# Kernel optimization log

Hardware: AMD Instinct MI355X
Metric: run time of the kernel (lower is better)

Reference implementation:

```python
import jax, jax.numpy as jnp
import numpy as np

B, S, D = 4, 2048, 512

def setup_inputs() -> dict:
    key = jax.random.key(0)
    ks = jax.random.split(key, 7)
    # scale weights so unscaled logits stay in a sane softmax range
    w_scale = 0.05
    return {
        "x": jax.random.normal(ks[0], (B, S, D), dtype=jnp.float32),
        "W_q": jax.random.normal(ks[1], (D, D), dtype=jnp.float32) * w_scale,
        "W_k": jax.random.normal(ks[2], (D, D), dtype=jnp.float32) * w_scale,
        "W_v": jax.random.normal(ks[3], (D, D), dtype=jnp.float32) * w_scale,
        "b_q": jax.random.normal(ks[4], (D,), dtype=jnp.float32) * w_scale,
        "b_k": jax.random.normal(ks[5], (D,), dtype=jnp.float32) * w_scale,
        "b_v": jax.random.normal(ks[6], (D,), dtype=jnp.float32) * w_scale,
    }

def reference(x, W_q, W_k, W_v, b_q, b_k, b_v):
    # QKV projections: [B,S,D] @ [D,D] + [D]
    q = jnp.einsum('bsd,de->bse', x, W_q) + b_q
    k = jnp.einsum('bsd,de->bse', x, W_k) + b_k
    v = jnp.einsum('bsd,de->bse', x, W_v) + b_v
    # unscaled attention scores [B,S,S]
    scores = jnp.einsum('bqd,bkd->bqk', q, k)
    attn = jax.nn.softmax(scores, axis=-1)
    # weighted sum of values [B,S,D]
    return jnp.einsum('bqk,bkd->bqd', attn, v)
```

## Files before the change

kernel.cpp:

```cpp
#include <hip/hip_runtime.h>
#include <hip/hip_bf16.h>
#include <hip/hip_fp16.h>

#define BB 4
#define SS 2048
#define DD 512

typedef short s16x8 __attribute__((ext_vector_type(8)));
typedef short s16x4 __attribute__((ext_vector_type(4)));
typedef float f32x4 __attribute__((ext_vector_type(4)));
typedef _Float16 f16x8 __attribute__((ext_vector_type(8)));

__device__ __forceinline__ short f2h(float f) {
    const _Float16 h = (_Float16)f;
    union { _Float16 h; short s; } u; u.h = h; return u.s;
}
__device__ __forceinline__ f16x8 as_h(s16x8 v) {
    union { s16x8 s; f16x8 h; } u; u.s = v; return u.h;
}

__device__ __forceinline__ void gload_lds16(const void* g, void* l) {
    __builtin_amdgcn_global_load_lds(
        (const __attribute__((address_space(1))) void*)g,
        (__attribute__((address_space(3))) void*)l, 16, 0, 0);
}

#define SB0 __builtin_amdgcn_sched_barrier(0)
#define LGKM0 asm volatile("s_waitcnt lgkmcnt(0)" ::: "memory")
#define VM0   asm volatile("s_waitcnt vmcnt(0)" ::: "memory")

__global__ __launch_bounds__(256, 4) void qkt128(
    const short* __restrict__ qf, const short* __restrict__ kf,
    short* __restrict__ outS, int nwg)
{
    __shared__ short lds[16384];

    const int tid = threadIdx.x;
    const int wave = tid >> 6, lane = tid & 63;
    const int flat = blockIdx.x + 16 * blockIdx.y + 256 * blockIdx.z;
    const int w = (flat & 7) * (nwg >> 3) + (flat >> 3);
    const int bm = ((w >> 4) & 15) * 128, bn = (w & 15) * 128;
    const long z = w >> 8;
    qf += z * (long)SS * DD; kf += z * (long)SS * DD;
    outS += z * (long)SS * SS;

    const int wm = (wave >> 1) * 64, wn = (wave & 1) * 64;
    const int lrow = lane & 15, lk16 = (lane >> 4) * 16;

    f32x4 acc[4][4] = {};

    auto base = [&](int buf, int arr) -> short* { return &lds[(buf * 2 + arr) * 4096]; };
    auto issue = [&](int buf, int arr, int k0) {
#pragma unroll
        for (int h = 0; h < 2; h++) {
            const int Lb = (h << 12) + (tid << 4);
            const int Ls = Lb ^ (((Lb >> 7) & 3) << 4);
            const int row = Ls >> 6, elem = (Ls & 63) >> 1;
            const short* s = arr ? kf : qf;
            const int rb = arr ? bn : bm;
            gload_lds16(s + (size_t)(rb + row) * DD + k0 + elem,
                        (char*)base(buf, arr) + Lb);
        }
    };
    auto rd = [&](int buf, int arr, int row) -> s16x8 {
        const int L = (row << 6) + lk16;
        const int Ls = L ^ (((L >> 7) & 3) << 4);
        return *(const s16x8*)((const char*)base(buf, arr) + Ls);
    };

#define QK_TILE(T, CUR, PREF)                                                    \
  {                                                                              \
    s16x8 a[4], b[4];                                                            \
    _Pragma("unroll")                                                            \
    for (int m = 0; m < 4; m++) a[m] = rd(CUR, 0, wm + m * 16 + lrow);           \
    _Pragma("unroll")                                                            \
    for (int n = 0; n < 4; n++) b[n] = rd(CUR, 1, wn + n * 16 + lrow);           \
    if (PREF) { issue((CUR) ^ 1, 1, ((T) + 1) * 32); SB0;                        \
                issue((CUR) ^ 1, 0, ((T) + 1) * 32); }                           \
    LGKM0; SB0;                                                                  \
    __builtin_amdgcn_s_setprio(1);                                               \
    _Pragma("unroll")                                                            \
    for (int m = 0; m < 4; m++) {                                                \
      _Pragma("unroll")                                                          \
      for (int n = 0; n < 4; n++)                                                \
        acc[m][n] = __builtin_amdgcn_mfma_f32_16x16x32_f16(                      \
            as_h(a[m]), as_h(b[n]), acc[m][n], 0, 0, 0);                         \
    }                                                                            \
    __builtin_amdgcn_s_setprio(0);                                               \
    if (PREF) { VM0; SB0; }                                                      \
    __builtin_amdgcn_s_barrier();                                                \
  }

    issue(0, 1, 0); issue(0, 0, 0);
    VM0;
    __builtin_amdgcn_s_barrier();

    for (int t = 0; t < 16; t += 2) {
        QK_TILE(t,     0, 1);
        QK_TILE(t + 1, 1, (t + 1) < 15);
    }
#undef QK_TILE

    __syncthreads();
    short* ebuf = &lds[0];
#pragma unroll
    for (int m = 0; m < 4; m++) {
#pragma unroll
        for (int n = 0; n < 4; n++) {
#pragma unroll
            for (int j = 0; j < 4; j++) {
                const int rl = wm + m * 16 + (lane >> 4) * 4 + j;
                const int cl = wn + n * 16 + lrow;
                ebuf[rl * 128 + (cl ^ ((rl & 7) << 3))] =
                    (short)__float2int_rn(acc[m][n][j] * 128.0f);
            }
        }
    }
    __syncthreads();
#pragma unroll
    for (int it = 0; it < 8; it++) {
        const int u = it * 256 + tid;
        const int r = u >> 4, c8 = (u & 15) * 8;
        const s16x8 val = *(const s16x8*)&ebuf[r * 128 + (c8 ^ ((r & 7) << 3))];
        *(s16x8*)&outS[(size_t)(bm + r) * SS + bn + c8] = val;
    }
}

__global__ __launch_bounds__(256, 4) void proj_all(
    const short* __restrict__ xh, const short* __restrict__ wt,
    const float* __restrict__ bq, const float* __restrict__ bk,
    const float* __restrict__ bv,
    short* __restrict__ qfp, short* __restrict__ kfp, short* __restrict__ vt)
{
    __shared__ short lds[16384];

    const int tid = threadIdx.x;
    const int wave = tid >> 6, lane = tid & 63;
    const int flat = blockIdx.x + 12 * blockIdx.y;
    const int w = (flat & 7) * 96 + (flat >> 3);
    const int bxi = w % 12, byi = w / 12;
    const int wsel = bxi >> 2;
    const int bnl = (bxi & 3) * 128;
    const int bm = byi * 128;
    const short* B0 = wt + (size_t)wsel * DD * DD;
    const float* bias = (wsel == 0) ? bq : (wsel == 1) ? bk : bv;

    f32x4 acc[4][4] = {};
    const int wm = (wave >> 1) * 64, wn = (wave & 1) * 64;
    const int lrow = lane & 15, lk16 = (lane >> 4) * 16;

    auto base = [&](int buf, int arr) -> short* { return &lds[(buf * 2 + arr) * 4096]; };
    auto issue = [&](int buf, int arr, int k0) {
#pragma unroll
        for (int h = 0; h < 2; h++) {
            const int Lb = (h << 12) + (tid << 4);
            const int Ls = Lb ^ (((Lb >> 7) & 3) << 4);
            const int row = Ls >> 6, elem = (Ls & 63) >> 1;
            const short* s = arr ? B0 : xh;
            const int rb = arr ? bnl : bm;
            gload_lds16(s + (size_t)(rb + row) * DD + k0 + elem,
                        (char*)base(buf, arr) + Lb);
        }
    };
    auto rd = [&](int buf, int arr, int row) -> s16x8 {
        const int L = (row << 6) + lk16;
        const int Ls = L ^ (((L >> 7) & 3) << 4);
        return *(const s16x8*)((const char*)base(buf, arr) + Ls);
    };

#define PJ_TILE(T, CUR, PREF)                                                    \
  {                                                                              \
    s16x8 a[4], b[4];                                                            \
    _Pragma("unroll")                                                            \
    for (int m = 0; m < 4; m++) a[m] = rd(CUR, 0, wm + m * 16 + lrow);           \
    _Pragma("unroll")                                                            \
    for (int n = 0; n < 4; n++) b[n] = rd(CUR, 1, wn + n * 16 + lrow);           \
    if (PREF) { issue((CUR) ^ 1, 1, ((T) + 1) * 32); SB0;                        \
                issue((CUR) ^ 1, 0, ((T) + 1) * 32); }                           \
    LGKM0; SB0;                                                                  \
    __builtin_amdgcn_s_setprio(1);                                               \
    _Pragma("unroll")                                                            \
    for (int m = 0; m < 4; m++) {                                                \
      _Pragma("unroll")                                                          \
      for (int n = 0; n < 4; n++)                                                \
        acc[m][n] = __builtin_amdgcn_mfma_f32_16x16x32_f16(                      \
            as_h(a[m]), as_h(b[n]), acc[m][n], 0, 0, 0);                         \
    }                                                                            \
    __builtin_amdgcn_s_setprio(0);                                               \
    if (PREF) { VM0; SB0; }                                                      \
    __builtin_amdgcn_s_barrier();                                                \
  }

    issue(0, 1, 0); issue(0, 0, 0);
    VM0;
    __builtin_amdgcn_s_barrier();

    for (int t = 0; t < 16; t += 2) {
        PJ_TILE(t,     0, 1);
        PJ_TILE(t + 1, 1, (t + 1) < 15);
    }
#undef PJ_TILE

    __syncthreads();
    short* cbuf = &lds[0];
#pragma unroll
    for (int m = 0; m < 4; m++) {
#pragma unroll
        for (int n = 0; n < 4; n++) {
#pragma unroll
            for (int j = 0; j < 4; j++) {
                const int rl = wm + m * 16 + (lane >> 4) * 4 + j;
                const int cl = wn + n * 16 + lrow;
                const float v = acc[m][n][j] + bias[bnl + cl];
                if (wsel < 2)
                    cbuf[rl * 128 + (cl ^ ((rl & 7) << 3))] = f2h(v);
                else
                    cbuf[cl * 128 + (rl ^ ((cl & 7) << 3))] = f2h(v);
            }
        }
    }
    __syncthreads();
    if (wsel < 2) {
        short* outp = wsel ? kfp : qfp;
#pragma unroll
        for (int it = 0; it < 8; it++) {
            const int u = it * 256 + tid;
            const int r = u >> 4, c8 = (u & 15) * 8;
            const s16x8 val = *(const s16x8*)&cbuf[r * 128 + (c8 ^ ((r & 7) << 3))];
            *(s16x8*)&outp[(size_t)(bm + r) * DD + bnl + c8] = val;
        }
    } else {
        const int b = bm >> 11, s0 = bm & 2047;
#pragma unroll
        for (int it = 0; it < 8; it++) {
            const int idx = it * 256 + tid;
            const int dd = idx >> 4, c8 = (idx & 15) * 8;
            const s16x8 val = *(const s16x8*)&cbuf[dd * 128 + (c8 ^ ((dd & 7) << 3))];
            *(s16x8*)&vt[((size_t)b << 20) + ((size_t)(bnl + dd) << 11) + s0 + c8] = val;
        }
    }
}

__global__ __launch_bounds__(256, 3) void pv_gemm(
    const short* __restrict__ P, const short* __restrict__ vt,
    float* __restrict__ out, int nwg)
{
    __shared__ short As[2][64 * 64];
    __shared__ short Bs[2][128 * 64];

    const int tid = threadIdx.x;
    const int wave = tid >> 6, lane = tid & 63;
    const int flat = blockIdx.x + 4 * blockIdx.y + 128 * blockIdx.z;
    const int w = (flat & 7) * (nwg >> 3) + (flat >> 3);
    const int bm = ((w >> 2) & 31) * 64, bn = (w & 3) * 128;
    const long z = w >> 7;
    P += z * (long)SS * SS;
    vt += z << 20;
    out += z * (long)SS * DD;

    f32x4 acc[2][4] = {};
    const int wm = (wave >> 1) * 32, wn = (wave & 1) * 64;
    const int lrow = lane & 15, lk = (lane >> 4) * 8;

    auto swz = [](int L) { return L ^ (((L >> 7) & 7) << 4); };
    auto issueA = [&](int buf, int k0) {
#pragma unroll
        for (int h = 0; h < 2; h++) {
            const int L = (h << 12) + (tid << 4);
            const int Ls = swz(L);
            const int row = Ls >> 7, col = (Ls & 127) >> 1;
            gload_lds16(P + (size_t)(bm + row) * SS + k0 + col, (char*)&As[buf][0] + L);
        }
    };
    auto issueB = [&](int buf, int k0) {
#pragma unroll
        for (int h = 0; h < 4; h++) {
            const int L = (h << 12) + (tid << 4);
            const int Ls = swz(L);
            const int row = Ls >> 7, col = (Ls & 127) >> 1;
            gload_lds16(vt + ((size_t)(bn + row) << 11) + k0 + col, (char*)&Bs[buf][0] + L);
        }
    };

#define PV_TILE(T, CUR, PREF)                                                    \
  {                                                                              \
    s16x8 a[2][2], b[2][4];                                                      \
    _Pragma("unroll")                                                            \
    for (int kx = 0; kx < 2; kx++) {                                             \
      _Pragma("unroll")                                                          \
      for (int m = 0; m < 2; m++)                                                \
        a[kx][m] = *(const s16x8*)((const char*)&As[CUR][0] +                    \
                   swz(((wm + m * 16 + lrow) * 64 + kx * 32 + lk) * 2));         \
      _Pragma("unroll")                                                          \
      for (int n = 0; n < 4; n++)                                                \
        b[kx][n] = *(const s16x8*)((const char*)&Bs[CUR][0] +                    \
                   swz(((wn + n * 16 + lrow) * 64 + kx * 32 + lk) * 2));         \
    }                                                                            \
    if (PREF) { issueB((CUR) ^ 1, ((T) + 1) * 64); SB0;                          \
                issueA((CUR) ^ 1, ((T) + 1) * 64); }                             \
    LGKM0; SB0;                                                                  \
    __builtin_amdgcn_s_setprio(1);                                               \
    _Pragma("unroll")                                                            \
    for (int kx = 0; kx < 2; kx++) {                                             \
      _Pragma("unroll")                                                          \
      for (int m = 0; m < 2; m++) {                                              \
        _Pragma("unroll")                                                        \
        for (int n = 0; n < 4; n++)                                              \
          acc[m][n] = __builtin_amdgcn_mfma_f32_16x16x32_f16(                    \
              as_h(a[kx][m]), as_h(b[kx][n]), acc[m][n], 0, 0, 0);               \
      }                                                                          \
    }                                                                            \
    __builtin_amdgcn_s_setprio(0);                                               \
    if (PREF) { VM0; SB0; }                                                      \
    __builtin_amdgcn_s_barrier();                                                \
  }

    issueB(0, 0); issueA(0, 0);
    VM0;
    __builtin_amdgcn_s_barrier();

    for (int t = 0; t < 32; t += 2) {
        PV_TILE(t,     0, 1);
        PV_TILE(t + 1, 1, (t + 1) < 31);
    }
#undef PV_TILE

#pragma unroll
    for (int m = 0; m < 2; m++) {
#pragma unroll
        for (int n = 0; n < 4; n++) {
#pragma unroll
            for (int j = 0; j < 4; j++) {
                const int row = bm + wm + m * 16 + (lane >> 4) * 4 + j;
                const int col = bn + wn + n * 16 + lrow;
                out[(size_t)row * DD + col] = acc[m][n][j];
            }
        }
    }
}

__global__ __launch_bounds__(256) void cast_all(
    const float* __restrict__ x,
    const float* __restrict__ wq, const float* __restrict__ wk,
    const float* __restrict__ wv,
    short* __restrict__ xh, short* __restrict__ wt)
{
    const int bid = blockIdx.x;
    if (bid < 4096) {
        const int i = bid * 256 + threadIdx.x;
        const float4 v = ((const float4*)x)[i];
        const float vv[4] = {v.x, v.y, v.z, v.w};
        s16x4 h;
#pragma unroll
        for (int j = 0; j < 4; j++) h[j] = f2h(vv[j]);
        ((s16x4*)xh)[i] = h;
    } else {
        const int t = (bid - 4096) * 256 + threadIdx.x;
        const int w = t >> 18;
        const int r = t & 262143;
        const float* src = (w == 0) ? wq : ((w == 1) ? wk : wv);
        const float v = src[r];
        const int k = r >> 9, n = r & 511;
        wt[((size_t)w << 18) + ((size_t)n << 9) + k] = f2h(v);
    }
}

__global__ __launch_bounds__(256) void softmax_rows(
    const short* __restrict__ S, short* __restrict__ P)
{
    const int row = blockIdx.x;
    const long z = blockIdx.y;
    const short* s = S + z * (long)SS * SS + (long)row * SS;
    short* p = P + z * (long)SS * SS + (long)row * SS;
    const int tid = threadIdx.x;

    const s16x8 raw = ((const s16x8*)s)[tid];
    float v[8];
#pragma unroll
    for (int j = 0; j < 8; j++) v[j] = (float)(int)raw[j] * 0.0078125f;

    float m = v[0];
#pragma unroll
    for (int j = 1; j < 8; j++) m = fmaxf(m, v[j]);
#pragma unroll
    for (int off = 32; off >= 1; off >>= 1) m = fmaxf(m, __shfl_xor(m, off));
    __shared__ float redm[4], reds[4];
    if ((tid & 63) == 0) redm[tid >> 6] = m;
    __syncthreads();
    m = fmaxf(fmaxf(redm[0], redm[1]), fmaxf(redm[2], redm[3]));

    float e[8], sum = 0.f;
#pragma unroll
    for (int j = 0; j < 8; j++) { e[j] = __expf(v[j] - m); sum += e[j]; }
#pragma unroll
    for (int off = 32; off >= 1; off >>= 1) sum += __shfl_xor(sum, off);
    if ((tid & 63) == 0) reds[tid >> 6] = sum;
    __syncthreads();
    sum = reds[0] + reds[1] + reds[2] + reds[3];
    const float inv = 1.0f / sum;

    s16x8 o;
#pragma unroll
    for (int j = 0; j < 8; j++) o[j] = f2h(e[j] * inv);
    ((s16x8*)p)[tid] = o;
}

extern "C" void kernel_launch(void* const* d_in, const int* in_sizes, int n_in,
                              void* d_out, int out_size, void* d_ws, size_t ws_size,
                              hipStream_t stream)
{
    const float* x  = (const float*)d_in[0];
    const float* Wq = (const float*)d_in[1];
    const float* Wk = (const float*)d_in[2];
    const float* Wv = (const float*)d_in[3];
    const float* bq = (const float*)d_in[4];
    const float* bk = (const float*)d_in[5];
    const float* bv = (const float*)d_in[6];
    float* out = (float*)d_out;

    const size_t MK = (size_t)BB * SS * DD;
    char* ws = (char*)d_ws;
    short* xh  = (short*)ws; ws += MK * 2;
    short* wt  = (short*)ws; ws += 3ull * DD * DD * 2;
    short* qfp = (short*)ws; ws += MK * 2;
    short* kfp = (short*)ws; ws += MK * 2;
    short* vt  = (short*)ws; ws += MK * 2;
    const size_t fixed = (size_t)(ws - (char*)d_ws);

    int g = 4;
    while (g > 0 && fixed + (size_t)g * ((size_t)SS * SS * 2 + (size_t)SS * SS * 2) > ws_size)
        g >>= 1;
    if (g == 0) return;
    short* sc = (short*)ws;
    short* P  = (short*)(ws + (size_t)g * SS * SS * 2);

    cast_all<<<dim3(7168), 256, 0, stream>>>(x, Wq, Wk, Wv, xh, wt);
    proj_all<<<dim3(12, 64), 256, 0, stream>>>(xh, wt, bq, bk, bv,
                                               qfp, kfp, vt);

    for (int b0 = 0; b0 < BB; b0 += g) {
        const int gg = (b0 + g <= BB) ? g : (BB - b0);
        qkt128<<<dim3(16, 16, gg), 256, 0, stream>>>(
            qfp + (size_t)b0 * SS * DD, kfp + (size_t)b0 * SS * DD, sc, 256 * gg);
        softmax_rows<<<dim3(SS, gg), 256, 0, stream>>>(sc, P);
        pv_gemm<<<dim3(4, 32, gg), 256, 0, stream>>>(
            P, vt + ((size_t)b0 << 20), out + (size_t)b0 * SS * DD, 128 * gg);
    }
}
```

Before: 100.9 us.

## Triple-buffer LDS tiles in QK^T and projection GEMMs with prefetch depth two

Both GEMM kernels move from double to triple buffering of the LDS tiles. Each step now issues global-to-LDS loads two k-tiles ahead and waits with vmcnt(4) rather than draining all outstanding loads, so global memory latency can hide behind more MFMA work. This grows LDS per block from 32KB to 48KB and lowers the launch-bounds occupancy hint from 4 to 3 blocks per CU, so fewer blocks can overlap on each CU.

```diff
diff --git a/kernel.cpp b/kernel.cpp
--- a/kernel.cpp
+++ b/kernel.cpp
@@ -28,12 +28,13 @@
 #define SB0 __builtin_amdgcn_sched_barrier(0)
 #define LGKM0 asm volatile("s_waitcnt lgkmcnt(0)" ::: "memory")
 #define VM0   asm volatile("s_waitcnt vmcnt(0)" ::: "memory")
-
-__global__ __launch_bounds__(256, 4) void qkt128(
+#define VM4   asm volatile("s_waitcnt vmcnt(4)" ::: "memory")
+
+__global__ __launch_bounds__(256, 3) void qkt128(
     const short* __restrict__ qf, const short* __restrict__ kf,
     short* __restrict__ outS, int nwg)
 {
-    __shared__ short lds[16384];
+    __shared__ short lds[24576];
 
     const int tid = threadIdx.x;
     const int wave = tid >> 6, lane = tid & 63;
@@ -68,15 +69,15 @@
         return *(const s16x8*)((const char*)base(buf, arr) + Ls);
     };
 
-#define QK_TILE(T, CUR, PREF)                                                    \
+#define QK_TILE(T, CUR, NX2)                                                     \
   {                                                                              \
     s16x8 a[4], b[4];                                                            \
     _Pragma("unroll")                                                            \
     for (int m = 0; m < 4; m++) a[m] = rd(CUR, 0, wm + m * 16 + lrow);           \
     _Pragma("unroll")                                                            \
     for (int n = 0; n < 4; n++) b[n] = rd(CUR, 1, wn + n * 16 + lrow);           \
-    if (PREF) { issue((CUR) ^ 1, 1, ((T) + 1) * 32); SB0;                        \
-                issue((CUR) ^ 1, 0, ((T) + 1) * 32); }                           \
+    if ((T) + 2 < 16) { issue(NX2, 1, ((T) + 2) * 32); SB0;                      \
+                        issue(NX2, 0, ((T) + 2) * 32); }                         \
     LGKM0; SB0;                                                                  \
     __builtin_amdgcn_s_setprio(1);                                               \
     _Pragma("unroll")                                                            \
@@ -87,18 +88,24 @@
             as_h(a[m]), as_h(b[n]), acc[m][n], 0, 0, 0);                         \
     }                                                                            \
     __builtin_amdgcn_s_setprio(0);                                               \
-    if (PREF) { VM0; SB0; }                                                      \
+    if ((T) < 15) {                                                              \
+      if ((T) + 2 < 16) { VM4; } else { VM0; }                                   \
+      SB0;                                                                       \
+    }                                                                            \
     __builtin_amdgcn_s_barrier();                                                \
   }
 
-    issue(0, 1, 0); issue(0, 0, 0);
-    VM0;
+    issue(0, 1, 0);  issue(0, 0, 0);
+    issue(1, 1, 32); issue(1, 0, 32);
+    VM4;
     __builtin_amdgcn_s_barrier();
 
-    for (int t = 0; t < 16; t += 2) {
-        QK_TILE(t,     0, 1);
-        QK_TILE(t + 1, 1, (t + 1) < 15);
-    }
+    for (int t = 0; t < 15; t += 3) {
+        QK_TILE(t,     0, 2);
+        QK_TILE(t + 1, 1, 0);
+        QK_TILE(t + 2, 2, 1);
+    }
+    QK_TILE(15, 0, 2);
 #undef QK_TILE
 
     __syncthreads();
@@ -126,13 +133,13 @@
     }
 }
 
-__global__ __launch_bounds__(256, 4) void proj_all(
+__global__ __launch_bounds__(256, 3) void proj_all(
     const short* __restrict__ xh, const short* __restrict__ wt,
     const float* __restrict__ bq, const float* __restrict__ bk,
     const float* __restrict__ bv,
     short* __restrict__ qfp, short* __restrict__ kfp, short* __restrict__ vt)
 {
-    __shared__ short lds[16384];
+    __shared__ short lds[24576];
 
     const int tid = threadIdx.x;
     const int wave = tid >> 6, lane = tid & 63;
@@ -168,15 +175,15 @@
         return *(const s16x8*)((const char*)base(buf, arr) + Ls);
     };
 
-#define PJ_TILE(T, CUR, PREF)                                                    \
+#define PJ_TILE(T, CUR, NX2)                                                     \
   {                                                                              \
     s16x8 a[4], b[4];                                                            \
     _Pragma("unroll")                                                            \
     for (int m = 0; m < 4; m++) a[m] = rd(CUR, 0, wm + m * 16 + lrow);           \
     _Pragma("unroll")                                                            \
     for (int n = 0; n < 4; n++) b[n] = rd(CUR, 1, wn + n * 16 + lrow);           \
-    if (PREF) { issue((CUR) ^ 1, 1, ((T) + 1) * 32); SB0;                        \
-                issue((CUR) ^ 1, 0, ((T) + 1) * 32); }                           \
+    if ((T) + 2 < 16) { issue(NX2, 1, ((T) + 2) * 32); SB0;                      \
+                        issue(NX2, 0, ((T) + 2) * 32); }                         \
     LGKM0; SB0;                                                                  \
     __builtin_amdgcn_s_setprio(1);                                               \
     _Pragma("unroll")                                                            \
@@ -187,18 +194,24 @@
             as_h(a[m]), as_h(b[n]), acc[m][n], 0, 0, 0);                         \
     }                                                                            \
     __builtin_amdgcn_s_setprio(0);                                               \
-    if (PREF) { VM0; SB0; }                                                      \
+    if ((T) < 15) {                                                              \
+      if ((T) + 2 < 16) { VM4; } else { VM0; }                                   \
+      SB0;                                                                       \
+    }                                                                            \
     __builtin_amdgcn_s_barrier();                                                \
   }
 
-    issue(0, 1, 0); issue(0, 0, 0);
-    VM0;
+    issue(0, 1, 0);  issue(0, 0, 0);
+    issue(1, 1, 32); issue(1, 0, 32);
+    VM4;
     __builtin_amdgcn_s_barrier();
 
-    for (int t = 0; t < 16; t += 2) {
-        PJ_TILE(t,     0, 1);
-        PJ_TILE(t + 1, 1, (t + 1) < 15);
-    }
+    for (int t = 0; t < 15; t += 3) {
+        PJ_TILE(t,     0, 2);
+        PJ_TILE(t + 1, 1, 0);
+        PJ_TILE(t + 2, 2, 1);
+    }
+    PJ_TILE(15, 0, 2);
 #undef PJ_TILE
 
     __syncthreads();
```

Result: no change. 99.72 us (-1.2%).
